# Optimization experiments

Hardware: AMD Instinct MI355X
Metric: run time of the kernel (lower is better)

The kernel has to match this reference:

```python
import jax, jax.numpy as jnp
import numpy as np

HID = 128  # hidden_dim

def _run_layer(x, W, b):
    """x: [B,T,Cin,H,W]; W: [4*HID, Cin+HID] (gate order i,f,o,g); b: [4*HID]."""
    B, T, Cin, H, Wd = x.shape
    h0 = jnp.zeros((B, HID, H, Wd), x.dtype)
    c0 = jnp.zeros_like(h0)
    xt = jnp.moveaxis(x, 1, 0)  # [T,B,Cin,H,W]

    def step(carry, x_t):
        h, c = carry
        z = jnp.concatenate([x_t, h], axis=1)                     # [B,Cin+HID,H,W]
        gates = jnp.einsum('bchw,gc->bghw', z, W) + b[None, :, None, None]
        i, f, o, g = jnp.split(gates, 4, axis=1)                  # each [B,HID,H,W]
        c_n = jax.nn.sigmoid(f) * c + jax.nn.sigmoid(i) * jnp.tanh(g)
        h_n = jax.nn.sigmoid(o) * jnp.tanh(c_n)
        return (h_n, c_n), h_n

    (hT, cT), hs = jax.lax.scan(step, (h0, c0), xt)
    return jnp.moveaxis(hs, 0, 1), hT, cT  # [B,T,HID,H,W], [B,HID,H,W] x2


def setup_inputs() -> dict:
    key = jax.random.key(0)
    ks = jax.random.split(key, 5)
    B, T, Cin, H, W = 8, 32, 64, 32, 32
    x = jax.random.normal(ks[0], (B, T, Cin, H, W), dtype=jnp.float32)
    W0 = jax.random.normal(ks[1], (4 * HID, Cin + HID), dtype=jnp.float32) * 0.05
    b0 = jax.random.normal(ks[2], (4 * HID,), dtype=jnp.float32) * 0.05
    W1 = jax.random.normal(ks[3], (4 * HID, HID + HID), dtype=jnp.float32) * 0.05
    b1 = jax.random.normal(ks[4], (4 * HID,), dtype=jnp.float32) * 0.05
    return {"x": x, "W0": W0, "b0": b0, "W1": W1, "b1": b1}


def reference(x, W0, b0, W1, b1):
    y0, _, _ = _run_layer(x, W0, b0)      # layer 0
    y1, hT, cT = _run_layer(y0, W1, b1)   # layer 1 (last layer)
    return y1, hT, cT
```

## Files before the change

kernel.cpp:

```cpp
#include <hip/hip_runtime.h>

typedef short bf16x8 __attribute__((ext_vector_type(8)));
typedef short bf16x4 __attribute__((ext_vector_type(4)));
typedef float f32x4  __attribute__((ext_vector_type(4)));
typedef unsigned int u32x2 __attribute__((ext_vector_type(2)));

#define HID 128
#define TT 32
#define HWSZ 1024
#define PX 32
#define NTHREADS 512

__device__ __forceinline__ unsigned short f2bf(float f) {
    union { float f; unsigned int i; } v; v.f = f;
    unsigned int u = v.i;
    return (unsigned short)((u + 0x7fffu + ((u >> 16) & 1u)) >> 16);
}
__device__ __forceinline__ unsigned int cvt_pk_bf16(float lo, float hi) {
    unsigned int r;
    asm("v_cvt_pk_bf16_f32 %0, %1, %2" : "=v"(r) : "v"(lo), "v"(hi));
    return r;
}
__device__ __forceinline__ float frcp(float x) { return __builtin_amdgcn_rcpf(x); }
__device__ __forceinline__ float sigm(float x) { return frcp(1.0f + __expf(-x)); }
__device__ __forceinline__ float ftanh(float x){ return 1.0f - 2.0f * frcp(1.0f + __expf(2.0f * x)); }

template <int CIN, bool FINAL, bool IN_LOCAL, bool OUT_LOCAL>
__global__ __launch_bounds__(NTHREADS, 2)
void lstm_layer(const void* __restrict__ in_, const float* __restrict__ W,
                const float* __restrict__ bias, void* __restrict__ y_,
                float* __restrict__ hT, float* __restrict__ cT)
{
    constexpr int K      = CIN + HID;
    constexpr int XK     = CIN / 32;
    constexpr int HK     = HID / 32;
    constexpr int KITERS = K / 32;
    constexpr int HB0 = 3 * CIN, HB1 = 3 * CIN + HID;
    constexpr int PITCH = 3 * CIN + 2 * HID + 8;
    constexpr int NIT = (PX * CIN / 4) / NTHREADS;

    const float* inF          = (const float*)in_;
    const unsigned short* inL = (const unsigned short*)in_;
    float* yF                 = (float*)y_;
    unsigned short* yL        = (unsigned short*)y_;

    __shared__ __align__(16) unsigned short z[PX][PITCH];

    const int tid  = threadIdx.x;
    const int wave = tid >> 6;
    const int lane = tid & 63;
    const int q    = lane >> 4;
    const int ln   = lane & 15;

    const int p0  = blockIdx.x * PX;
    const int b   = p0 >> 10;
    const int hw0 = p0 & 1023;

    const long long locbase = (long long)blockIdx.x * TT * PX * HID;
    const long long inFbase = (long long)b * TT * CIN * HWSZ + hw0;

    bf16x8 Af[KITERS][4];
    #pragma unroll
    for (int k = 0; k < KITERS; ++k) {
        #pragma unroll
        for (int g = 0; g < 4; ++g) {
            const float* wp = W + (g * HID + wave * 16 + ln) * K + k * 32 + q * 8;
            bf16x8 v;
            #pragma unroll
            for (int j = 0; j < 8; ++j) v[j] = (short)f2bf(wp[j]);
            Af[k][g] = v;
        }
    }
    f32x4 bs[4];
    #pragma unroll
    for (int g = 0; g < 4; ++g)
        bs[g] = *(const f32x4*)(bias + g * HID + wave * 16 + q * 4);

    const int ch0 = wave * 16 + q * 4;
    float* const ybase = yF + ((long long)b * TT * HID + ch0) * HWSZ + hw0;

    #pragma unroll
    for (int idx = tid; idx < PX * HID; idx += NTHREADS)
        z[idx & (PX - 1)][HB0 + (idx >> 5)] = 0;
    if (IN_LOCAL) {
        bf16x8 v0 = *(const bf16x8*)(inL + locbase + tid * 8);
        bf16x8 v1 = *(const bf16x8*)(inL + locbase + (long long)PX * HID + tid * 8);
        *(bf16x8*)&z[tid >> 4][(tid & 15) * 8] = v0;
        *(bf16x8*)&z[tid >> 4][CIN + (tid & 15) * 8] = v1;
    } else {
        #pragma unroll
        for (int it = 0; it < NIT; ++it) {
            const int idx = tid + it * NTHREADS;
            const int pxs = idx & 31, c0 = (idx >> 5) * 4;
            float a0[4], a1[4];
            #pragma unroll
            for (int j = 0; j < 4; ++j) a0[j] = inF[inFbase + (c0 + j) * HWSZ + pxs];
            #pragma unroll
            for (int j = 0; j < 4; ++j) a1[j] = inF[inFbase + (long long)CIN * HWSZ + (c0 + j) * HWSZ + pxs];
            u32x2 v0, v1;
            v0[0] = cvt_pk_bf16(a0[0], a0[1]); v0[1] = cvt_pk_bf16(a0[2], a0[3]);
            v1[0] = cvt_pk_bf16(a1[0], a1[1]); v1[1] = cvt_pk_bf16(a1[2], a1[3]);
            *(u32x2*)&z[pxs][c0] = v0;
            *(u32x2*)&z[pxs][CIN + c0] = v1;
        }
    }
    __syncthreads();

    float cst[2][4];
    #pragma unroll
    for (int mt = 0; mt < 2; ++mt)
        #pragma unroll
        for (int r = 0; r < 4; ++r) cst[mt][r] = 0.0f;

    f32x4 accA[2][4], accB[2][4];
    #pragma unroll
    for (int g = 0; g < 4; ++g) { accA[0][g] = bs[g]; accA[1][g] = bs[g]; }
    #pragma unroll
    for (int k = 0; k < XK; ++k) {
        const int koff = k * 32;
        const bf16x8 pv0 = *(const bf16x8*)&z[ln][koff + q * 8];
        const bf16x8 pv1 = *(const bf16x8*)&z[16 + ln][koff + q * 8];
        #pragma unroll
        for (int g = 0; g < 4; ++g) {
            accA[0][g] = __builtin_amdgcn_mfma_f32_16x16x32_bf16(Af[k][g], pv0, accA[0][g], 0, 0, 0);
            accA[1][g] = __builtin_amdgcn_mfma_f32_16x16x32_bf16(Af[k][g], pv1, accA[1][g], 0, 0, 0);
        }
    }

#define LSTM_STEP(T, PAR, ACCC, ACCN)                                            \
    {                                                                            \
        const int hb_r = (PAR) ? HB1 : HB0;                                      \
        const int hb_w = (PAR) ? HB0 : HB1;                                      \
        const int xs_n = ((T) + 1) % 3;                                          \
        const int xs_w = ((T) + 2) % 3;                                          \
        const int tn2  = ((T) + 2 < TT) ? (T) + 2 : TT - 1;                      \
        bf16x8 pfv; float pff[NIT][4];                                           \
        if (IN_LOCAL) {                                                          \
            pfv = *(const bf16x8*)(inL + locbase + (long long)tn2 * PX * HID + tid * 8); \
        } else {                                                                 \
            _Pragma("unroll")                                                    \
            for (int it = 0; it < NIT; ++it) {                                   \
                const int idx = tid + it * NTHREADS;                             \
                const int pxs = idx & 31, c0 = (idx >> 5) * 4;                   \
                _Pragma("unroll")                                                \
                for (int j = 0; j < 4; ++j)                                      \
                    pff[it][j] = inF[inFbase + (long long)tn2 * CIN * HWSZ + (c0 + j) * HWSZ + pxs]; \
            }                                                                    \
        }                                                                        \
        _Pragma("unroll")                                                        \
        for (int k = 0; k < HK; ++k) {                                           \
            const int koff = hb_r + k * 32;                                      \
            const bf16x8 pv0 = *(const bf16x8*)&z[ln][koff + q * 8];             \
            const bf16x8 pv1 = *(const bf16x8*)&z[16 + ln][koff + q * 8];        \
            _Pragma("unroll")                                                    \
            for (int g = 0; g < 4; ++g) {                                        \
                ACCC[0][g] = __builtin_amdgcn_mfma_f32_16x16x32_bf16(Af[XK + k][g], pv0, ACCC[0][g], 0, 0, 0); \
                ACCC[1][g] = __builtin_amdgcn_mfma_f32_16x16x32_bf16(Af[XK + k][g], pv1, ACCC[1][g], 0, 0, 0); \
            }                                                                    \
        }                                                                        \
        _Pragma("unroll")                                                        \
        for (int g = 0; g < 4; ++g) { ACCN[0][g] = bs[g]; ACCN[1][g] = bs[g]; }  \
        _Pragma("unroll")                                                        \
        for (int k = 0; k < XK; ++k) {                                           \
            const int koff = xs_n * CIN + k * 32;                                \
            const bf16x8 pv0 = *(const bf16x8*)&z[ln][koff + q * 8];             \
            const bf16x8 pv1 = *(const bf16x8*)&z[16 + ln][koff + q * 8];        \
            _Pragma("unroll")                                                    \
            for (int g = 0; g < 4; ++g) {                                        \
                ACCN[0][g] = __builtin_amdgcn_mfma_f32_16x16x32_bf16(Af[k][g], pv0, ACCN[0][g], 0, 0, 0); \
                ACCN[1][g] = __builtin_amdgcn_mfma_f32_16x16x32_bf16(Af[k][g], pv1, ACCN[1][g], 0, 0, 0); \
            }                                                                    \
        }                                                                        \
        _Pragma("unroll")                                                        \
        for (int mt = 0; mt < 2; ++mt) {                                         \
            const int px = mt * 16 + ln;                                         \
            float hr[4];                                                         \
            _Pragma("unroll")                                                    \
            for (int r = 0; r < 4; ++r) {                                        \
                const float iv = sigm(ACCC[mt][0][r]);                           \
                const float fv = sigm(ACCC[mt][1][r]);                           \
                const float ov = sigm(ACCC[mt][2][r]);                           \
                const float gv = ftanh(ACCC[mt][3][r]);                          \
                const float c  = fv * cst[mt][r] + iv * gv;                      \
                cst[mt][r] = c;                                                  \
                hr[r] = ov * ftanh(c);                                           \
                if (FINAL && (T) == TT - 1)                                      \
                    cT[((long long)(b * HID + ch0 + r)) * HWSZ + hw0 + px] = c;  \
            }                                                                    \
            u32x2 hv;                                                            \
            hv[0] = cvt_pk_bf16(hr[0], hr[1]);                                   \
            hv[1] = cvt_pk_bf16(hr[2], hr[3]);                                   \
            *(u32x2*)&z[px][hb_w + ch0] = hv;                                    \
            if (FINAL || !OUT_LOCAL) {                                           \
                float* yp = ybase + (long long)(T) * (HID * HWSZ) + px;          \
                yp[0] = hr[0]; yp[HWSZ] = hr[1];                                 \
                yp[2 * HWSZ] = hr[2]; yp[3 * HWSZ] = hr[3];                      \
                if (FINAL && (T) == TT - 1) {                                    \
                    float* hp = hT + ((long long)(b * HID + ch0)) * HWSZ + hw0 + px; \
                    hp[0] = hr[0]; hp[HWSZ] = hr[1];                             \
                    hp[2 * HWSZ] = hr[2]; hp[3 * HWSZ] = hr[3];                  \
                }                                                                \
            }                                                                    \
        }                                                                        \
        if (IN_LOCAL) {                                                          \
            *(bf16x8*)&z[tid >> 4][xs_w * CIN + (tid & 15) * 8] = pfv;           \
        } else {                                                                 \
            _Pragma("unroll")                                                    \
            for (int it = 0; it < NIT; ++it) {                                   \
                const int idx = tid + it * NTHREADS;                             \
                const int pxs = idx & 31, c0 = (idx >> 5) * 4;                   \
                u32x2 xv;                                                        \
                xv[0] = cvt_pk_bf16(pff[it][0], pff[it][1]);                     \
                xv[1] = cvt_pk_bf16(pff[it][2], pff[it][3]);                     \
                *(u32x2*)&z[pxs][xs_w * CIN + c0] = xv;                          \
            }                                                                    \
        }                                                                        \
        asm volatile("s_waitcnt lgkmcnt(0)\n\ts_barrier" ::: "memory");          \
        if (!FINAL && OUT_LOCAL) {                                               \
            bf16x8 hv8 = *(const bf16x8*)&z[tid >> 4][hb_w + (tid & 15) * 8];    \
            *(bf16x8*)(yL + locbase + (long long)(T) * PX * HID + tid * 8) = hv8; \
        }                                                                        \
    }

    for (int t = 0; t < TT; t += 2) {
        LSTM_STEP(t,     0, accA, accB)
        LSTM_STEP(t + 1, 1, accB, accA)
    }
#undef LSTM_STEP
}

extern "C" void kernel_launch(void* const* d_in, const int* in_sizes, int n_in,
                              void* d_out, int out_size, void* d_ws, size_t ws_size,
                              hipStream_t stream) {
    const float* x  = (const float*)d_in[0];
    const float* W0 = (const float*)d_in[1];
    const float* b0 = (const float*)d_in[2];
    const float* W1 = (const float*)d_in[3];
    const float* b1 = (const float*)d_in[4];
    float* out = (float*)d_out;

    float* y  = out;
    float* hT = out + 33554432;
    float* cT = out + 34603008;

    dim3 grid(8192 / PX), block(NTHREADS);

    const size_t y0_bytes = (size_t)8 * HWSZ * TT * HID * 2;
    if (ws_size >= y0_bytes) {
        unsigned short* y0 = (unsigned short*)d_ws;
        lstm_layer<64,  false, false, true ><<<grid, block, 0, stream>>>(x,  W0, b0, y0, nullptr, nullptr);
        lstm_layer<128, true,  true,  false><<<grid, block, 0, stream>>>(y0, W1, b1, y,  hT, cT);
    } else {
        lstm_layer<64,  false, false, false><<<grid, block, 0, stream>>>(x, W0, b0, y, nullptr, nullptr);
        lstm_layer<128, true,  false, false><<<grid, block, 0, stream>>>(y, W1, b1, y, hT, cT);
    }
}
```

Baseline: 364.6 us.

## Stagger wave schedules across halves and fuse LSTM activations with shared reciprocals

```diff
diff --git a/kernel.cpp b/kernel.cpp
--- a/kernel.cpp
+++ b/kernel.cpp
@@ -1,7 +1,6 @@
 #include <hip/hip_runtime.h>
 
 typedef short bf16x8 __attribute__((ext_vector_type(8)));
-typedef short bf16x4 __attribute__((ext_vector_type(4)));
 typedef float f32x4  __attribute__((ext_vector_type(4)));
 typedef unsigned int u32x2 __attribute__((ext_vector_type(2)));
 
@@ -22,8 +21,8 @@
     return r;
 }
 __device__ __forceinline__ float frcp(float x) { return __builtin_amdgcn_rcpf(x); }
-__device__ __forceinline__ float sigm(float x) { return frcp(1.0f + __expf(-x)); }
-__device__ __forceinline__ float ftanh(float x){ return 1.0f - 2.0f * frcp(1.0f + __expf(2.0f * x)); }
+
+#define BARRIER() asm volatile("s_waitcnt lgkmcnt(0)\n\ts_barrier" ::: "memory")
 
 template <int CIN, bool FINAL, bool IN_LOCAL, bool OUT_LOCAL>
 __global__ __launch_bounds__(NTHREADS, 2)
@@ -31,10 +30,9 @@
                 const float* __restrict__ bias, void* __restrict__ y_,
                 float* __restrict__ hT, float* __restrict__ cT)
 {
-    constexpr int K      = CIN + HID;
-    constexpr int XK     = CIN / 32;
-    constexpr int HK     = HID / 32;
-    constexpr int KITERS = K / 32;
+    constexpr int XK  = CIN / 32;
+    constexpr int HK  = HID / 32;
+    constexpr int KITERS = XK + HK;
     constexpr int HB0 = 3 * CIN, HB1 = 3 * CIN + HID;
     constexpr int PITCH = 3 * CIN + 2 * HID + 8;
     constexpr int NIT = (PX * CIN / 4) / NTHREADS;
@@ -64,7 +62,7 @@
     for (int k = 0; k < KITERS; ++k) {
         #pragma unroll
         for (int g = 0; g < 4; ++g) {
-            const float* wp = W + (g * HID + wave * 16 + ln) * K + k * 32 + q * 8;
+            const float* wp = W + (g * HID + wave * 16 + ln) * (CIN + HID) + k * 32 + q * 8;
             bf16x8 v;
             #pragma unroll
             for (int j = 0; j < 8; ++j) v[j] = (short)f2bf(wp[j]);
@@ -127,14 +125,10 @@
         }
     }
 
-#define LSTM_STEP(T, PAR, ACCC, ACCN)                                            \
-    {                                                                            \
-        const int hb_r = (PAR) ? HB1 : HB0;                                      \
-        const int hb_w = (PAR) ? HB0 : HB1;                                      \
-        const int xs_n = ((T) + 1) % 3;                                          \
-        const int xs_w = ((T) + 2) % 3;                                          \
-        const int tn2  = ((T) + 2 < TT) ? (T) + 2 : TT - 1;                      \
-        bf16x8 pfv; float pff[NIT][4];                                           \
+#define PREFETCH(T)                                                              \
+    bf16x8 pfv; float pff[NIT][4];                                               \
+    {                                                                            \
+        const int tn2 = ((T) + 2 < TT) ? (T) + 2 : TT - 1;                       \
         if (IN_LOCAL) {                                                          \
             pfv = *(const bf16x8*)(inL + locbase + (long long)tn2 * PX * HID + tid * 8); \
         } else {                                                                 \
@@ -147,6 +141,11 @@
                     pff[it][j] = inF[inFbase + (long long)tn2 * CIN * HWSZ + (c0 + j) * HWSZ + pxs]; \
             }                                                                    \
         }                                                                        \
+    }
+
+#define HMFMA(ACCC, PAR)                                                         \
+    {                                                                            \
+        const int hb_r = (PAR) ? HB1 : HB0;                                      \
         _Pragma("unroll")                                                        \
         for (int k = 0; k < HK; ++k) {                                           \
             const int koff = hb_r + k * 32;                                      \
@@ -158,6 +157,11 @@
                 ACCC[1][g] = __builtin_amdgcn_mfma_f32_16x16x32_bf16(Af[XK + k][g], pv1, ACCC[1][g], 0, 0, 0); \
             }                                                                    \
         }                                                                        \
+    }
+
+#define XMFMA(ACCN, T)                                                           \
+    {                                                                            \
+        const int xs_n = ((T) + 1) % 3;                                          \
         _Pragma("unroll")                                                        \
         for (int g = 0; g < 4; ++g) { ACCN[0][g] = bs[g]; ACCN[1][g] = bs[g]; }  \
         _Pragma("unroll")                                                        \
@@ -171,19 +175,31 @@
                 ACCN[1][g] = __builtin_amdgcn_mfma_f32_16x16x32_bf16(Af[k][g], pv1, ACCN[1][g], 0, 0, 0); \
             }                                                                    \
         }                                                                        \
+    }
+
+#define PWB(ACCC, T, PAR)                                                        \
+    {                                                                            \
+        __builtin_amdgcn_s_setprio(1);                                           \
+        const int hb_w = (PAR) ? HB0 : HB1;                                      \
         _Pragma("unroll")                                                        \
         for (int mt = 0; mt < 2; ++mt) {                                         \
             const int px = mt * 16 + ln;                                         \
             float hr[4];                                                         \
             _Pragma("unroll")                                                    \
             for (int r = 0; r < 4; ++r) {                                        \
-                const float iv = sigm(ACCC[mt][0][r]);                           \
-                const float fv = sigm(ACCC[mt][1][r]);                           \
-                const float ov = sigm(ACCC[mt][2][r]);                           \
-                const float gv = ftanh(ACCC[mt][3][r]);                          \
-                const float c  = fv * cst[mt][r] + iv * gv;                      \
+                const float ei = __expf(-ACCC[mt][0][r]);                        \
+                const float ef = __expf(-ACCC[mt][1][r]);                        \
+                const float eo = __expf(-ACCC[mt][2][r]);                        \
+                const float eg = __expf(-2.0f * ACCC[mt][3][r]);                 \
+                const float a1 = 1.0f + ei;                                      \
+                const float a2 = 1.0f + eg;                                      \
+                const float a3 = 1.0f + ef;                                      \
+                const float p12 = a1 * a2;                                       \
+                const float num = cst[mt][r] * p12 + (1.0f - eg) * a3;           \
+                const float c   = num * frcp(a3 * p12);                          \
                 cst[mt][r] = c;                                                  \
-                hr[r] = ov * ftanh(c);                                           \
+                const float ec = __expf(-2.0f * c);                              \
+                hr[r] = (1.0f - ec) * frcp((1.0f + eo) * (1.0f + ec));           \
                 if (FINAL && (T) == TT - 1)                                      \
                     cT[((long long)(b * HID + ch0 + r)) * HWSZ + hw0 + px] = c;  \
             }                                                                    \
@@ -202,6 +218,12 @@
                 }                                                                \
             }                                                                    \
         }                                                                        \
+        __builtin_amdgcn_s_setprio(0);                                           \
+    }
+
+#define XWRITE(T)                                                                \
+    {                                                                            \
+        const int xs_w = ((T) + 2) % 3;                                          \
         if (IN_LOCAL) {                                                          \
             *(bf16x8*)&z[tid >> 4][xs_w * CIN + (tid & 15) * 8] = pfv;           \
         } else {                                                                 \
@@ -215,18 +237,42 @@
                 *(u32x2*)&z[pxs][xs_w * CIN + c0] = xv;                          \
             }                                                                    \
         }                                                                        \
-        asm volatile("s_waitcnt lgkmcnt(0)\n\ts_barrier" ::: "memory");          \
-        if (!FINAL && OUT_LOCAL) {                                               \
-            bf16x8 hv8 = *(const bf16x8*)&z[tid >> 4][hb_w + (tid & 15) * 8];    \
-            *(bf16x8*)(yL + locbase + (long long)(T) * PX * HID + tid * 8) = hv8; \
-        }                                                                        \
-    }
-
-    for (int t = 0; t < TT; t += 2) {
-        LSTM_STEP(t,     0, accA, accB)
-        LSTM_STEP(t + 1, 1, accB, accA)
-    }
-#undef LSTM_STEP
+    }
+
+#define YEMIT(T, PAR)                                                            \
+    if (!FINAL && OUT_LOCAL) {                                                   \
+        const int hb_w = (PAR) ? HB0 : HB1;                                      \
+        bf16x8 hv8 = *(const bf16x8*)&z[tid >> 4][hb_w + (tid & 15) * 8];        \
+        *(bf16x8*)(yL + locbase + (long long)(T) * PX * HID + tid * 8) = hv8;    \
+    }
+
+#define STEP_HFIRST(T, PAR, ACCC, ACCN)                                          \
+    { PREFETCH(T) HMFMA(ACCC, PAR) PWB(ACCC, T, PAR) XMFMA(ACCN, T)              \
+      XWRITE(T) BARRIER(); YEMIT(T, PAR) }
+
+#define STEP_XFIRST(T, PAR, ACCC, ACCN)                                          \
+    { PREFETCH(T) XMFMA(ACCN, T) HMFMA(ACCC, PAR) PWB(ACCC, T, PAR)              \
+      XWRITE(T) BARRIER(); YEMIT(T, PAR) }
+
+    if (((wave >> 2) & 1) == 0) {
+        for (int t = 0; t < TT; t += 2) {
+            STEP_HFIRST(t,     0, accA, accB)
+            STEP_HFIRST(t + 1, 1, accB, accA)
+        }
+    } else {
+        for (int t = 0; t < TT; t += 2) {
+            STEP_XFIRST(t,     0, accA, accB)
+            STEP_XFIRST(t + 1, 1, accB, accA)
+        }
+    }
+#undef PREFETCH
+#undef HMFMA
+#undef XMFMA
+#undef PWB
+#undef XWRITE
+#undef YEMIT
+#undef STEP_HFIRST
+#undef STEP_XFIRST
 }
 
 extern "C" void kernel_launch(void* const* d_in, const int* in_sizes, int n_in,
```

After: 344.6 us. 5.5% less time.
